# Optimization experiments

Measured on AMD Instinct MI355X. Metric: run time of the kernel, lower is better.

## Reference

```python
import jax, jax.numpy as jnp
import numpy as np

V, E, H, M = 256, 512, 512, 128
D = 2 * H  # decoder hidden
B, L_TXT, T_MEL = 32, 256, 800
EPS = 1e-5


def setup_inputs() -> dict:
    key = jax.random.key(0)
    ks = jax.random.split(key, 24)
    s = 0.02
    inp = {
        'x': jax.random.randint(ks[0], (B, L_TXT), 0, V),
        'text_seq_lens': jax.random.randint(ks[1], (B,), 1, L_TXT + 1),
        'y': jax.random.normal(ks[2], (B, T_MEL, M), jnp.float32),
        'mel_spec_lens': jax.random.randint(ks[3], (B,), 1, T_MEL + 1),
        'emb': jax.random.normal(ks[4], (V, E)) * s,
        'conv1_w': jax.random.normal(ks[5], (E, E, 3)) * s,
        'conv1_b': jnp.zeros((E,)),
        'bn1_g': jnp.ones((E,)), 'bn1_b': jnp.zeros((E,)),
        'conv2_w': jax.random.normal(ks[6], (E, E, 3)) * s,
        'conv2_b': jnp.zeros((E,)),
        'bn2_g': jnp.ones((E,)), 'bn2_b': jnp.zeros((E,)),
        'wih_f': jax.random.normal(ks[7], (4 * H, E)) * s,
        'whh_f': jax.random.normal(ks[8], (4 * H, H)) * s,
        'bih_f': jnp.zeros((4 * H,)), 'bhh_f': jnp.zeros((4 * H,)),
        'wih_b': jax.random.normal(ks[9], (4 * H, E)) * s,
        'whh_b': jax.random.normal(ks[10], (4 * H, H)) * s,
        'bih_b': jnp.zeros((4 * H,)), 'bhh_b': jnp.zeros((4 * H,)),
        'dwih': jax.random.normal(ks[11], (4 * D, M)) * s,
        'dwhh': jax.random.normal(ks[12], (4 * D, D)) * s,
        'dbih': jnp.zeros((4 * D,)), 'dbhh': jnp.zeros((4 * D,)),
        'proj_w': jax.random.normal(ks[13], (M, D)) * s,
        'proj_b': jnp.zeros((M,)),
        'gate_w': jax.random.normal(ks[14], (1, D)) * s,
        'gate_b': jnp.zeros((1,)),
    }
    return inp


def _conv_bn_relu(x, w, b, g, beta):
    # x: (B, E, L); training-mode BatchNorm (batch statistics, biased var)
    x = jax.lax.conv_general_dilated(x, w, (1,), [(1, 1)],
                                     dimension_numbers=('NCH', 'OIH', 'NCH')) + b[None, :, None]
    mu = jnp.mean(x, axis=(0, 2), keepdims=True)
    var = jnp.mean((x - mu) ** 2, axis=(0, 2), keepdims=True)
    x = (x - mu) * jax.lax.rsqrt(var + EPS) * g[None, :, None] + beta[None, :, None]
    return jax.nn.relu(x)


def _lstm_last(xseq, lens, wih, whh, bih, bhh):
    # Run LSTM over full padded seq, freezing state past each length.
    # Returns final (h, c) == state at t = len-1 (packed-sequence semantics).
    Bb, T, _ = xseq.shape
    Hh = whh.shape[1]
    pre = jnp.einsum('bte,ge->btg', xseq, wih) + bih + bhh  # (B,T,4H)

    def step(carry, inp):
        h, c = carry
        xt, t = inp
        gates = xt + h @ whh.T
        i, f, g, o = jnp.split(gates, 4, axis=-1)
        c_n = jax.nn.sigmoid(f) * c + jax.nn.sigmoid(i) * jnp.tanh(g)
        h_n = jax.nn.sigmoid(o) * jnp.tanh(c_n)
        valid = (t < lens)[:, None]
        return (jnp.where(valid, h_n, h), jnp.where(valid, c_n, c)), None

    init = (jnp.zeros((Bb, Hh), xseq.dtype), jnp.zeros((Bb, Hh), xseq.dtype))
    (h, c), _ = jax.lax.scan(step, init, (pre.transpose(1, 0, 2), jnp.arange(T)))
    return h, c


def _forward(x, text_seq_lens, y, mel_spec_lens, emb, conv1_w, conv1_b, bn1_g, bn1_b,
             conv2_w, conv2_b, bn2_g, bn2_b, wih_f, whh_f, bih_f, bhh_f,
             wih_b, whh_b, bih_b, bhh_b, dwih, dwhh, dbih, dbhh,
             proj_w, proj_b, gate_w, gate_b):
    xe = emb[x]                       # (B, L, E)
    h = xe.transpose(0, 2, 1)         # (B, E, L)
    h = _conv_bn_relu(h, conv1_w, conv1_b, bn1_g, bn1_b)  # dropout = identity (eval)
    h = _conv_bn_relu(h, conv2_w, conv2_b, bn2_g, bn2_b)
    h = h.transpose(0, 2, 1)          # (B, L, E)

    # bidirectional encoder LSTM final states (packed semantics)
    hf, cf = _lstm_last(h, text_seq_lens, wih_f, whh_f, bih_f, bhh_f)
    # reverse each sequence within its valid length for the backward direction
    t_idx = jnp.arange(h.shape[1])[None, :]
    rev_idx = jnp.clip(text_seq_lens[:, None] - 1 - t_idx, 0, h.shape[1] - 1)
    h_rev = jnp.take_along_axis(h, rev_idx[:, :, None], axis=1)
    hb, cb = _lstm_last(h_rev, text_seq_lens, wih_b, whh_b, bih_b, bhh_b)

    hid = jnp.concatenate([hf, hb], axis=1)  # (B, 2H)
    cel = jnp.concatenate([cf, cb], axis=1)

    Tm = y.shape[1]

    def dec_step(carry, _):
        hd, cd, inp = carry
        gates = inp @ dwih.T + dbih + dbhh + hd @ dwhh.T
        i, f, g, o = jnp.split(gates, 4, axis=-1)
        cd = jax.nn.sigmoid(f) * cd + jax.nn.sigmoid(i) * jnp.tanh(g)
        hd = jax.nn.sigmoid(o) * jnp.tanh(cd)
        mel = hd @ proj_w.T + proj_b          # (B, M)
        gate = hd @ gate_w.T + gate_b         # (B, 1)
        return (hd, cd, mel), (mel, gate[:, 0])

    sos = jnp.zeros((y.shape[0], M), y.dtype)
    _, (mels, gates) = jax.lax.scan(dec_step, (hid, cel, sos), None, length=Tm)
    mel_outputs = mels.transpose(1, 0, 2)     # (B, Tm, M)
    gate_outputs = gates.T                    # (B, Tm)

    mask = jnp.arange(Tm)[None, :] > mel_spec_lens[:, None]  # (B, Tm), strictly >
    masked_mel = jnp.where(mask[:, :, None], 0.0, mel_outputs)
    masked_gate = jnp.where(mask, 1000.0, gate_outputs)
    return masked_mel, masked_gate, mask


def reference(x, text_seq_lens, y, mel_spec_lens, emb, conv1_w, conv1_b, bn1_g, bn1_b,
              conv2_w, conv2_b, bn2_g, bn2_b, wih_f, whh_f, bih_f, bhh_f,
              wih_b, whh_b, bih_b, bhh_b, dwih, dwhh, dbih, dbhh,
              proj_w, proj_b, gate_w, gate_b):
    return _forward(x, text_seq_lens, y, mel_spec_lens, emb, conv1_w, conv1_b,
                    bn1_g, bn1_b, conv2_w, conv2_b, bn2_g, bn2_b,
                    wih_f, whh_f, bih_f, bhh_f, wih_b, whh_b, bih_b, bhh_b,
                    dwih, dwhh, dbih, dbhh, proj_w, proj_b, gate_w, gate_b)
```

## Files before the change

### kernel.cpp

```cpp
#include <hip/hip_runtime.h>


typedef float f4 __attribute__((ext_vector_type(4)));
typedef _Float16 h8 __attribute__((ext_vector_type(8)));
typedef _Float16 half_t;
typedef unsigned long long u64;

#define B_    32
#define LTXT  256
#define TMEL  800
#define EE    512
#define HH    512
#define DD    1024
#define MM    128
#define NROWS 8192
#define GATE_OFF 3276800
#define MASK_OFF 3302400

#define RING_D 801
#define RING_E 257
#define HOP    13

#define WS_MBE        0ull
#define WS_MBD        16384ull
#define WS_HENC       49152ull
#define WS_ZERO_BYTES 114688ull
#define WS_HD         16891904ull
#define WS_BUFX       69386240ull
#define WS_BUFY       77774848ull
#define WS_CONVF      86163456ull
#define WS_WEFF       86163456ull
#define WS_W0         94552064ull
#define WS_WP1        102940672ull
#define WS_WP2        104513536ull
#define WS_WIHP       106086400ull
#define WS_WHHP       110280704ull
#define WS_BSUM       114475008ull
#define WS_BEFF       114491392ull
#define WS_B0         114507776ull
#define WS_MEAN       114524160ull
#define WS_RSTD       114526208ull
#define WS_PROJW      114528256ull
#define WS_PROJG      114790400ull
#define WS_CEL        114823168ull

__device__ __forceinline__ float sigm(float x) { return 1.f / (1.f + __expf(-x)); }
__device__ __forceinline__ float tanh_f(float x) {
    float e = __expf(2.f * x);
    return 1.f - 2.f / (e + 1.f);
}

__device__ __forceinline__ void st_atom64(void* p, u64 v) {
    asm volatile("global_atomic_swap_x2 %0, %1, off" :: "v"(p), "v"(v) : "memory");
}
__device__ __forceinline__ void st_atom32(unsigned* p, unsigned v) {
    asm volatile("global_atomic_swap %0, %1, off" :: "v"(p), "v"(v) : "memory");
}


__global__ void k_embed(const int* __restrict__ x, const float* __restrict__ emb,
                        half_t* __restrict__ out) {
    int row = blockIdx.x;
    int tok = x[row];
    const float* e = emb + (size_t)tok * EE;
    half_t* o = out + (size_t)row * EE;
    for (int c = threadIdx.x; c < EE; c += blockDim.x) o[c] = (half_t)e[c];
}

__global__ void k_packconvw(const float* __restrict__ w, half_t* __restrict__ wp) {
    int idx = blockIdx.x * 256 + threadIdx.x;
    if (idx >= 3 * EE * EE) return;
    int s = idx / (EE * EE);
    int rem = idx - s * EE * EE;
    int eo = rem >> 9, ei = rem & 511;
    wp[idx] = (half_t)w[(size_t)eo * (EE * 3) + ei * 3 + s];
}

__global__ __launch_bounds__(256) void k_conv(const half_t* __restrict__ A,
                                              const half_t* __restrict__ Wp,
                                              const float* __restrict__ bias,
                                              float* __restrict__ out) {
    const int nt = blockIdx.x, et = blockIdx.y;
    const int tid = threadIdx.x;
    const int wv = tid >> 6, l = tid & 63, quad = l >> 4, lo = l & 15;
    const int rowA = nt * 64 + wv * 16 + lo;
    const int eo = et * 16 + lo;
    f4 acc = {0.f, 0.f, 0.f, 0.f};
    for (int s = 0; s < 3; ++s) {
        int lsp = (rowA & 255) + s - 1;
        bool valid = (lsp >= 0) && (lsp < 256);
        int rs = rowA + s - 1;
        rs = rs < 0 ? 0 : (rs > NROWS - 1 ? NROWS - 1 : rs);
        const half_t* ab = A + (size_t)rs * EE;
        const half_t* wb = Wp + ((size_t)s * EE + eo) * EE;
#pragma unroll 4
        for (int ks = 0; ks < 16; ++ks) {
            h8 a = {0, 0, 0, 0, 0, 0, 0, 0};
            if (valid) a = *(const h8*)(ab + ks * 32 + quad * 8);
            h8 b = *(const h8*)(wb + ks * 32 + quad * 8);
            acc = __builtin_amdgcn_mfma_f32_16x16x32_f16(a, b, acc, 0, 0, 0);
        }
    }
    const int orow = nt * 64 + wv * 16 + quad * 4;
    const float bv = bias[eo];
#pragma unroll
    for (int r = 0; r < 4; ++r) out[(size_t)(orow + r) * EE + eo] = acc[r] + bv;
}

__global__ __launch_bounds__(256) void k_bnstats(const float* __restrict__ x,
                                                 float* __restrict__ mean,
                                                 float* __restrict__ rstd) {
    const int c = blockIdx.x;
    float s = 0.f, ss = 0.f;
    for (int n = threadIdx.x; n < NROWS; n += 256) {
        float v = x[(size_t)n * EE + c];
        s += v; ss += v * v;
    }
#pragma unroll
    for (int off = 32; off > 0; off >>= 1) { s += __shfl_down(s, off); ss += __shfl_down(ss, off); }
    __shared__ float as[4], ass[4];
    int wv = threadIdx.x >> 6;
    if ((threadIdx.x & 63) == 0) { as[wv] = s; ass[wv] = ss; }
    __syncthreads();
    if (threadIdx.x == 0) {
        float S = as[0] + as[1] + as[2] + as[3];
        float SS = ass[0] + ass[1] + ass[2] + ass[3];
        float m = S / (float)NROWS;
        float var = SS / (float)NROWS - m * m;
        mean[c] = m;
        rstd[c] = rsqrtf(var + 1e-5f);
    }
}

__global__ void k_bnapply(const float* __restrict__ x, const float* __restrict__ mean,
                          const float* __restrict__ rstd, const float* __restrict__ g,
                          const float* __restrict__ beta, half_t* __restrict__ out) {
    int idx = blockIdx.x * 256 + threadIdx.x;
    if (idx >= NROWS * EE) return;
    int c = idx & (EE - 1);
    float v = (x[idx] - mean[c]) * rstd[c] * g[c] + beta[c];
    out[idx] = (half_t)(v > 0.f ? v : 0.f);
}

__global__ void k_packrec(const float* __restrict__ src, half_t* __restrict__ dst,
                          int Hdim, int kshift, int total) {
    int idx = blockIdx.x * 256 + threadIdx.x;
    if (idx >= total) return;
    int p = idx >> kshift;
    int k = idx & ((1 << kshift) - 1);
    int he = p >> 2, g = p & 3;
    dst[idx] = (half_t)src[((size_t)g * Hdim + he) * (size_t)(1 << kshift) + k];
}

__global__ void k_bsumenc(const float* __restrict__ bf, const float* __restrict__ bhf,
                          const float* __restrict__ bb, const float* __restrict__ bhb,
                          float* __restrict__ bsum) {
    int p = blockIdx.x * 256 + threadIdx.x;
    if (p >= 4096) return;
    int dir = p >> 11, pp = p & 2047;
    int he = pp >> 2, g = pp & 3;
    int row = g * HH + he;
    bsum[p] = dir ? (bb[row] + bhb[row]) : (bf[row] + bhf[row]);
}

__global__ __launch_bounds__(256) void k_weff(const float* __restrict__ dwhh,
                                              const float* __restrict__ dwih,
                                              const float* __restrict__ projw,
                                              half_t* __restrict__ weff,
                                              half_t* __restrict__ w0) {
    int row = blockIdx.x;
    int k = blockIdx.y * 256 + threadIdx.x;
    float v = dwhh[(size_t)row * DD + k];
    float acc = v;
    for (int m = 0; m < MM; ++m) acc += dwih[(size_t)row * MM + m] * projw[(size_t)m * DD + k];
    int p = ((row & (DD - 1)) << 2) | (row >> 10);
    weff[(size_t)p * DD + k] = (half_t)acc;
    w0[(size_t)p * DD + k] = (half_t)v;
}

__global__ void k_bdec(const float* __restrict__ dbih, const float* __restrict__ dbhh,
                       const float* __restrict__ dwih, const float* __restrict__ projb,
                       float* __restrict__ beff, float* __restrict__ b0) {
    int p = blockIdx.x * 256 + threadIdx.x;
    if (p >= 4096) return;
    int he = p >> 2, g = p & 3;
    int row = g * DD + he;
    float bb = dbih[row] + dbhh[row];
    float acc = bb;
    for (int m = 0; m < MM; ++m) acc += dwih[(size_t)row * MM + m] * projb[m];
    b0[p] = bb;
    beff[p] = acc;
}

__global__ void k_cast(const float* __restrict__ src, half_t* __restrict__ dst, int n) {
    int idx = blockIdx.x * 256 + threadIdx.x;
    if (idx < n) dst[idx] = (half_t)src[idx];
}

__global__ void k_projg(const float* __restrict__ gw, half_t* __restrict__ pg) {
    int idx = blockIdx.x * 256 + threadIdx.x;
    if (idx >= 16 * DD) return;
    int row = idx >> 10, k = idx & (DD - 1);
    pg[idx] = (half_t)(row == 0 ? gw[k] : 0.f);
}

__global__ void k_mask(const int* __restrict__ lens, float* __restrict__ out) {
    int idx = blockIdx.x * 256 + threadIdx.x;
    if (idx >= B_ * TMEL) return;
    int b = idx / TMEL, t = idx - b * TMEL;
    out[MASK_OFF + idx] = (t > lens[b]) ? 1.f : 0.f;
}

__global__ __launch_bounds__(512) void k_enc(const half_t* __restrict__ X,
                                             const half_t* __restrict__ wihp,
                                             const half_t* __restrict__ whhp,
                                             const float* __restrict__ bsum,
                                             const int* __restrict__ lens,
                                             half_t* __restrict__ henc,
                                             half_t* __restrict__ hd,
                                             float* __restrict__ cel,
                                             unsigned* __restrict__ mbE) {
    const int j = blockIdx.x;
    const int dir = j >> 5, sub = j & 31;
    const int tid = threadIdx.x;
    const int wv = tid >> 6, l = tid & 63, quad = l >> 4, lo = l & 15;
    const int rg = wv >> 1, bh = wv & 1;
    const int bfr = bh * 16 + lo;
    const int ue = tid >> 5, ub = tid & 31;

    __shared__ half_t s_hd[32 * 520];
    __shared__ float s_g[32][65];
    __shared__ float s_c[16][32];
    __shared__ float s_h[16][32];
    __shared__ half_t s_hh[16][32];
    __shared__ int s_len[32];

    if (tid < 32) s_len[tid] = lens[tid];
    s_c[ue][ub] = 0.f;
    s_h[ue][ub] = 0.f;

    const int pr = dir * 2048 + sub * 64 + rg * 16 + lo;
    const half_t* wih_b = wihp + (size_t)pr * 512;
    const half_t* whh_b = whhp + (size_t)pr * 512;
    const float bias_n = bsum[pr];

    h8 wihreg[16], whhreg[16];
#pragma unroll
    for (int ks = 0; ks < 16; ++ks) {
        wihreg[ks] = *(const h8*)(wih_b + ks * 32 + quad * 8);
        whhreg[ks] = *(const h8*)(whh_b + ks * 32 + quad * 8);
    }

    int sp = 0, sn = HOP;
    __syncthreads();

    for (int t = 0; t < 256; ++t) {
        if (t > 0) {
            if (tid >= 64 && tid < 96) {
                const unsigned want = (unsigned)t;
                const unsigned* fp = mbE + (size_t)(dir * 32 + sub) * 64 + (tid - 64);
                while (__hip_atomic_load(fp, __ATOMIC_RELAXED, __HIP_MEMORY_SCOPE_AGENT) < want)
                    __builtin_amdgcn_s_sleep(1);
            }
            __syncthreads();
        }

        const half_t* src = henc + (size_t)sp * 32768 + (size_t)dir * 16384;
        h8 tmp0 = *(const h8*)(src + (size_t)(tid + 0 * 512) * 8);
        h8 tmp1 = *(const h8*)(src + (size_t)(tid + 1 * 512) * 8);
        h8 tmp2 = *(const h8*)(src + (size_t)(tid + 2 * 512) * 8);
        h8 tmp3 = *(const h8*)(src + (size_t)(tid + 3 * 512) * 8);

        const int lb = s_len[bfr];
        int tt = (dir == 0) ? t : (lb - 1 - t);
        tt = tt < 0 ? 0 : tt;
        const half_t* xr = X + ((size_t)bfr * 256 + tt) * 512;
        f4 accA = {0.f, 0.f, 0.f, 0.f}, accB = {0.f, 0.f, 0.f, 0.f};
#pragma unroll
        for (int ks = 0; ks < 16; ++ks) {
            h8 a = *(const h8*)(xr + ks * 32 + quad * 8);
            accA = __builtin_amdgcn_mfma_f32_16x16x32_f16(a, wihreg[ks], accA, 0, 0, 0);
        }

        {
            int c0 = tid;
            *(h8*)(s_hd + (size_t)(c0 >> 6) * 520 + (c0 & 63) * 8) = tmp0;
            int c1 = tid + 512;
            *(h8*)(s_hd + (size_t)(c1 >> 6) * 520 + (c1 & 63) * 8) = tmp1;
            int c2 = tid + 1024;
            *(h8*)(s_hd + (size_t)(c2 >> 6) * 520 + (c2 & 63) * 8) = tmp2;
            int c3 = tid + 1536;
            *(h8*)(s_hd + (size_t)(c3 >> 6) * 520 + (c3 & 63) * 8) = tmp3;
        }
        __syncthreads();

#pragma unroll
        for (int ks = 0; ks < 16; ++ks) {
            h8 a = *(const h8*)(s_hd + (size_t)bfr * 520 + ks * 32 + quad * 8);
            accB = __builtin_amdgcn_mfma_f32_16x16x32_f16(a, whhreg[ks], accB, 0, 0, 0);
        }
        const int bm = bh * 16 + quad * 4, cm = rg * 16 + lo;
#pragma unroll
        for (int r = 0; r < 4; ++r) s_g[bm + r][cm] = accA[r] + accB[r] + bias_n;
        __syncthreads();
        {
            float gi = s_g[ub][ue * 4 + 0], gf = s_g[ub][ue * 4 + 1];
            float gg = s_g[ub][ue * 4 + 2], go = s_g[ub][ue * 4 + 3];
            float cn = sigm(gf) * s_c[ue][ub] + sigm(gi) * tanh_f(gg);
            float hn = sigm(go) * tanh_f(cn);
            if (t < s_len[ub]) { s_c[ue][ub] = cn; s_h[ue][ub] = hn; }
            s_hh[ue][ub] = (half_t)s_h[ue][ub];
        }
        __syncthreads();
        if (tid < 64 && t < 255) {
            int b2 = tid >> 1, e8 = (tid & 1) * 8;
            union { half_t h[8]; u64 u[2]; } pk;
#pragma unroll
            for (int i = 0; i < 8; ++i) pk.h[i] = s_hh[e8 + i][b2];
            half_t* dst = henc + (size_t)sn * 32768 + (size_t)dir * 16384
                          + (size_t)b2 * 512 + sub * 16 + e8;
            st_atom64(dst, pk.u[0]);
            st_atom64(dst + 4, pk.u[1]);
            asm volatile("s_waitcnt vmcnt(0)");
            if (tid < 32)
                st_atom32(mbE + ((size_t)(dir * 32 + tid) * 64 + sub), (unsigned)(t + 1));
        }
        if (t < 255) { sp = sn; sn += HOP; if (sn >= RING_E) sn -= RING_E; }
    }
    {
        int g2 = ub >> 4, b = ub & 15;
        hd[(size_t)g2 * ((size_t)RING_D * 16384) + (size_t)b * 1024
           + dir * 512 + sub * 16 + ue] = (half_t)s_h[ue][ub];
    }
    cel[(size_t)ub * 1024 + dir * 512 + sub * 16 + ue] = s_c[ue][ub];
}

__global__ __launch_bounds__(512) void k_dec(const half_t* __restrict__ Weff,
                                             const half_t* __restrict__ W0,
                                             const float* __restrict__ beff,
                                             const float* __restrict__ b0,
                                             const half_t* __restrict__ projwb,
                                             const half_t* __restrict__ projg,
                                             const float* __restrict__ projb,
                                             const float* __restrict__ gateb,
                                             const int* __restrict__ mlens,
                                             const float* __restrict__ cel,
                                             half_t* __restrict__ hd,
                                             float* __restrict__ out,
                                             unsigned* __restrict__ mbD) {
    const int j = blockIdx.x;
    const int tid = threadIdx.x;
    const int wv = tid >> 6, l = tid & 63, quad = l >> 4, lo = l & 15;

    __shared__ half_t s_hd[16 * 1032];
    __shared__ float s_g[16][129];
    __shared__ float s_c[32][16];
    __shared__ half_t s_hh[32][16];
    __shared__ int s_len[32];

    if (j < 64) {
        const int g = j >> 5, jj = j & 31;
        half_t* hdG = hd + (size_t)g * ((size_t)RING_D * 16384);
        unsigned* mbG = mbD + (size_t)g * 34 * 64;
        const int ue = tid >> 4;
        const int ub = tid & 15;

        s_c[ue][ub] = cel[(size_t)(g * 16 + ub) * 1024 + jj * 32 + ue];
        const int pr = jj * 128 + wv * 16 + lo;
        const float biasE = beff[pr], bias0 = b0[pr];
        const half_t* wbE = Weff + (size_t)pr * 1024;
        const half_t* wb0 = W0 + (size_t)pr * 1024;

        h8 wreg[32];
#pragma unroll
        for (int ks = 0; ks < 32; ++ks)
            wreg[ks] = *(const h8*)(wbE + ks * 32 + quad * 8);

        int sp = 0, sn = HOP;
        __syncthreads();

        for (int t = 1; t <= TMEL; ++t) {
            if (t > 1) {
                if (tid >= 64 && tid < 96) {
                    const unsigned want = (unsigned)(t - 1);
                    const unsigned* fp = mbG + (size_t)jj * 64 + (tid - 64);
                    while (__hip_atomic_load(fp, __ATOMIC_RELAXED, __HIP_MEMORY_SCOPE_AGENT) < want)
                        __builtin_amdgcn_s_sleep(1);
                }
                __syncthreads();
            }

            {
                const half_t* src = hdG + (size_t)sp * 16384;
                h8 tp[4];
#pragma unroll
                for (int i = 0; i < 4; ++i)
                    tp[i] = *(const h8*)(src + (size_t)(tid + i * 512) * 8);
#pragma unroll
                for (int i = 0; i < 4; ++i) {
                    int c = tid + i * 512;
                    *(h8*)(s_hd + (size_t)(c >> 7) * 1032 + (c & 127) * 8) = tp[i];
                }
            }
            __syncthreads();

            const half_t* ar = s_hd + (size_t)lo * 1032 + quad * 8;
            f4 acc = {0.f, 0.f, 0.f, 0.f}, acc2 = {0.f, 0.f, 0.f, 0.f};
            if (t == 1) {
#pragma unroll 8
                for (int ks = 0; ks < 32; ks += 2) {
                    h8 a0 = *(const h8*)(ar + ks * 32);
                    h8 a1 = *(const h8*)(ar + ks * 32 + 32);
                    acc = __builtin_amdgcn_mfma_f32_16x16x32_f16(a0, *(const h8*)(wb0 + ks * 32 + quad * 8), acc, 0, 0, 0);
                    acc2 = __builtin_amdgcn_mfma_f32_16x16x32_f16(a1, *(const h8*)(wb0 + ks * 32 + 32 + quad * 8), acc2, 0, 0, 0);
                }
            } else {
#pragma unroll
                for (int ks = 0; ks < 32; ks += 2) {
                    h8 a0 = *(const h8*)(ar + ks * 32);
                    h8 a1 = *(const h8*)(ar + ks * 32 + 32);
                    acc = __builtin_amdgcn_mfma_f32_16x16x32_f16(a0, wreg[ks], acc, 0, 0, 0);
                    acc2 = __builtin_amdgcn_mfma_f32_16x16x32_f16(a1, wreg[ks + 1], acc2, 0, 0, 0);
                }
            }
            const float bn = (t == 1) ? bias0 : biasE;
#pragma unroll
            for (int r = 0; r < 4; ++r) s_g[quad * 4 + r][wv * 16 + lo] = acc[r] + acc2[r] + bn;
            __syncthreads();
            {
                float gi = s_g[ub][ue * 4 + 0], gf = s_g[ub][ue * 4 + 1];
                float gg = s_g[ub][ue * 4 + 2], go = s_g[ub][ue * 4 + 3];
                float cn = sigm(gf) * s_c[ue][ub] + sigm(gi) * tanh_f(gg);
                s_c[ue][ub] = cn;
                s_hh[ue][ub] = (half_t)(sigm(go) * tanh_f(cn));
            }
            __syncthreads();
            if (tid < 64) {
                int b2 = tid >> 2, e8 = (tid & 3) * 8;
                union { half_t h[8]; u64 u[2]; } pk;
#pragma unroll
                for (int i = 0; i < 8; ++i) pk.h[i] = s_hh[e8 + i][b2];
                half_t* dst = hdG + (size_t)sn * 16384 + (size_t)b2 * 1024 + jj * 32 + e8;
                st_atom64(dst, pk.u[0]);
                st_atom64(dst + 4, pk.u[1]);
                asm volatile("s_waitcnt vmcnt(0)");
                if (tid < 34)
                    st_atom32(mbG + ((size_t)tid * 64 + jj), (unsigned)t);
            }
            sp = sn; sn += HOP; if (sn >= RING_D) sn -= RING_D;
        }
    } else {
        const int p = j - 64;
        const int g = p >> 1;
        const bool meld = ((p & 1) == 0);
        half_t* hdG = hd + (size_t)g * ((size_t)RING_D * 16384);
        unsigned* mbG = mbD + (size_t)g * 34 * 64;
        const int cons = meld ? 32 : 33;
        const bool duty = meld || (wv == 0);
        const half_t* pw = meld ? (projwb + (size_t)(wv * 16 + lo) * 1024)
                                : (projg + (size_t)lo * 1024);
        const float biasP = meld ? projb[wv * 16 + lo] : gateb[0];

        h8 pwreg[32];
        if (duty) {
#pragma unroll
            for (int ks = 0; ks < 32; ++ks)
                pwreg[ks] = *(const h8*)(pw + ks * 32 + quad * 8);
        }
        if (tid < 32) s_len[tid] = mlens[tid];

        int spP = HOP;
        __syncthreads();

        for (int t = 1; t <= TMEL; ++t) {
            if (tid < 32) {
                const unsigned want = (unsigned)t;
                const unsigned* fp = mbG + (size_t)cons * 64 + tid;
                while (__hip_atomic_load(fp, __ATOMIC_RELAXED, __HIP_MEMORY_SCOPE_AGENT) < want)
                    __builtin_amdgcn_s_sleep(1);
            }
            __syncthreads();

            {
                const half_t* src = hdG + (size_t)spP * 16384;
                h8 tp[4];
#pragma unroll
                for (int i = 0; i < 4; ++i)
                    tp[i] = *(const h8*)(src + (size_t)(tid + i * 512) * 8);
#pragma unroll
                for (int i = 0; i < 4; ++i) {
                    int c = tid + i * 512;
                    *(h8*)(s_hd + (size_t)(c >> 7) * 1032 + (c & 127) * 8) = tp[i];
                }
            }
            __syncthreads();

            if (duty) {
                const half_t* ar = s_hd + (size_t)lo * 1032 + quad * 8;
                f4 accm = {0.f, 0.f, 0.f, 0.f}, accm2 = {0.f, 0.f, 0.f, 0.f};
#pragma unroll
                for (int ks = 0; ks < 32; ks += 2) {
                    h8 a0 = *(const h8*)(ar + ks * 32);
                    h8 a1 = *(const h8*)(ar + ks * 32 + 32);
                    accm = __builtin_amdgcn_mfma_f32_16x16x32_f16(a0, pwreg[ks], accm, 0, 0, 0);
                    accm2 = __builtin_amdgcn_mfma_f32_16x16x32_f16(a1, pwreg[ks + 1], accm2, 0, 0, 0);
                }
                accm[0] += accm2[0]; accm[1] += accm2[1];
                accm[2] += accm2[2]; accm[3] += accm2[3];
                const int pos = t - 1;
                if (meld) {
#pragma unroll
                    for (int r = 0; r < 4; ++r) {
                        int b = g * 16 + quad * 4 + r;
                        float v = accm[r] + biasP;
                        if (pos > s_len[b]) v = 0.f;
                        __builtin_nontemporal_store(v,
                            &out[(size_t)b * (TMEL * MM) + (size_t)pos * MM + wv * 16 + lo]);
                    }
                } else if (lo == 0) {
#pragma unroll
                    for (int r = 0; r < 4; ++r) {
                        int b = g * 16 + quad * 4 + r;
                        float v = accm[r] + biasP;
                        if (pos > s_len[b]) v = 1000.f;
                        __builtin_nontemporal_store(v, &out[GATE_OFF + (size_t)b * TMEL + pos]);
                    }
                }
            }
            __syncthreads();
            spP += HOP; if (spP >= RING_D) spP -= RING_D;
        }
    }
}


extern "C" void kernel_launch(void* const* d_in, const int* in_sizes, int n_in,
                              void* d_out, int out_size, void* d_ws, size_t ws_size,
                              hipStream_t stream) {
    const int* x = (const int*)d_in[0];
    const int* tlens = (const int*)d_in[1];
    const int* mlens = (const int*)d_in[3];
    const float* emb = (const float*)d_in[4];
    const float* c1w = (const float*)d_in[5];
    const float* c1b = (const float*)d_in[6];
    const float* bn1g = (const float*)d_in[7];
    const float* bn1b = (const float*)d_in[8];
    const float* c2w = (const float*)d_in[9];
    const float* c2b = (const float*)d_in[10];
    const float* bn2g = (const float*)d_in[11];
    const float* bn2b = (const float*)d_in[12];
    const float* wihf = (const float*)d_in[13];
    const float* whhf = (const float*)d_in[14];
    const float* bihf = (const float*)d_in[15];
    const float* bhhf = (const float*)d_in[16];
    const float* wihb = (const float*)d_in[17];
    const float* whhb = (const float*)d_in[18];
    const float* bihb = (const float*)d_in[19];
    const float* bhhb = (const float*)d_in[20];
    const float* dwih = (const float*)d_in[21];
    const float* dwhh = (const float*)d_in[22];
    const float* dbih = (const float*)d_in[23];
    const float* dbhh = (const float*)d_in[24];
    const float* projw = (const float*)d_in[25];
    const float* projb = (const float*)d_in[26];
    const float* gatew = (const float*)d_in[27];
    const float* gateb = (const float*)d_in[28];
    float* out = (float*)d_out;
    char* ws = (char*)d_ws;

    unsigned* mbE = (unsigned*)(ws + WS_MBE);
    unsigned* mbD = (unsigned*)(ws + WS_MBD);
    half_t* henc = (half_t*)(ws + WS_HENC);
    half_t* hd = (half_t*)(ws + WS_HD);
    half_t* bufX = (half_t*)(ws + WS_BUFX);
    half_t* bufY = (half_t*)(ws + WS_BUFY);
    float* convf = (float*)(ws + WS_CONVF);
    half_t* weff = (half_t*)(ws + WS_WEFF);
    half_t* w0 = (half_t*)(ws + WS_W0);
    half_t* wp1 = (half_t*)(ws + WS_WP1);
    half_t* wp2 = (half_t*)(ws + WS_WP2);
    float* meanb = (float*)(ws + WS_MEAN);
    float* rstdb = (float*)(ws + WS_RSTD);
    half_t* wihp = (half_t*)(ws + WS_WIHP);
    half_t* whhp = (half_t*)(ws + WS_WHHP);
    float* bsum = (float*)(ws + WS_BSUM);
    float* beff = (float*)(ws + WS_BEFF);
    float* b0 = (float*)(ws + WS_B0);
    half_t* projwb = (half_t*)(ws + WS_PROJW);
    half_t* projg = (half_t*)(ws + WS_PROJG);
    float* cel = (float*)(ws + WS_CEL);

    hipMemsetAsync(d_ws, 0, (size_t)WS_ZERO_BYTES, stream);

    k_embed<<<NROWS, 256, 0, stream>>>(x, emb, bufX);
    k_packconvw<<<(3 * EE * EE + 255) / 256, 256, 0, stream>>>(c1w, wp1);
    k_conv<<<dim3(128, 32), 256, 0, stream>>>(bufX, wp1, c1b, convf);
    k_bnstats<<<EE, 256, 0, stream>>>(convf, meanb, rstdb);
    k_bnapply<<<(NROWS * EE) / 256, 256, 0, stream>>>(convf, meanb, rstdb, bn1g, bn1b, bufY);
    k_packconvw<<<(3 * EE * EE + 255) / 256, 256, 0, stream>>>(c2w, wp2);
    k_conv<<<dim3(128, 32), 256, 0, stream>>>(bufY, wp2, c2b, convf);
    k_bnstats<<<EE, 256, 0, stream>>>(convf, meanb, rstdb);
    k_bnapply<<<(NROWS * EE) / 256, 256, 0, stream>>>(convf, meanb, rstdb, bn2g, bn2b, bufX);

    const int encTot = 2048 * 512;
    k_packrec<<<(encTot + 255) / 256, 256, 0, stream>>>(wihf, wihp, HH, 9, encTot);
    k_packrec<<<(encTot + 255) / 256, 256, 0, stream>>>(wihb, wihp + encTot, HH, 9, encTot);
    k_packrec<<<(encTot + 255) / 256, 256, 0, stream>>>(whhf, whhp, HH, 9, encTot);
    k_packrec<<<(encTot + 255) / 256, 256, 0, stream>>>(whhb, whhp + encTot, HH, 9, encTot);
    k_bsumenc<<<16, 256, 0, stream>>>(bihf, bhhf, bihb, bhhb, bsum);

    k_enc<<<64, 512, 0, stream>>>(bufX, wihp, whhp, bsum, tlens, henc, hd, cel, mbE);

    k_weff<<<dim3(4096, 4), 256, 0, stream>>>(dwhh, dwih, projw, weff, w0);
    k_bdec<<<16, 256, 0, stream>>>(dbih, dbhh, dwih, projb, beff, b0);
    k_cast<<<(MM * DD + 255) / 256, 256, 0, stream>>>(projw, projwb, MM * DD);
    k_projg<<<(16 * DD + 255) / 256, 256, 0, stream>>>(gatew, projg);

    k_dec<<<68, 512, 0, stream>>>(weff, w0, beff, b0, projwb, projg, projb, gateb,
                                  mlens, cel, hd, out, mbD);

    k_mask<<<(B_ * TMEL + 255) / 256, 256, 0, stream>>>(mlens, out);

    (void)in_sizes; (void)n_in; (void)out_size; (void)ws_size;
}
```

Baseline: 4.482 ms.

## Split encoder LSTM blocks by batch half with wider hidden slices per block

The encoder recurrence now splits work across blocks by direction and batch half (16 sequences each), with each block owning 32 hidden units (128 gate rows) instead of 16 units for all 32 sequences. Each block copies half as much of the shared hidden state per step, and each block waits on 16 flags instead of 32. This cuts per-step cross-block synchronisation fan-in and global-to-LDS traffic. In exchange each wave holds a different weight-row slice, and the ring buffer and mailbox layout in workspace change, so k_dec and the host launch must agree with the new indexing.

Measured after the change: 4.464 ms. About the same (-0.4%).

```diff
diff --git a/kernel.cpp b/kernel.cpp
--- a/kernel.cpp
+++ b/kernel.cpp
@@ -221,25 +221,25 @@
                                              float* __restrict__ cel,
                                              unsigned* __restrict__ mbE) {
     const int j = blockIdx.x;
-    const int dir = j >> 5, sub = j & 31;
+    const int d = j >> 4, jj = j & 15;
+    const int dir = d >> 1, bg = d & 1;
     const int tid = threadIdx.x;
     const int wv = tid >> 6, l = tid & 63, quad = l >> 4, lo = l & 15;
-    const int rg = wv >> 1, bh = wv & 1;
-    const int bfr = bh * 16 + lo;
-    const int ue = tid >> 5, ub = tid & 31;
-
-    __shared__ half_t s_hd[32 * 520];
-    __shared__ float s_g[32][65];
-    __shared__ float s_c[16][32];
-    __shared__ float s_h[16][32];
-    __shared__ half_t s_hh[16][32];
-    __shared__ int s_len[32];
-
-    if (tid < 32) s_len[tid] = lens[tid];
+    const int ue = tid >> 4;
+    const int ub = tid & 15;
+
+    __shared__ half_t s_hd[16 * 520];
+    __shared__ float s_g[16][129];
+    __shared__ float s_c[32][16];
+    __shared__ float s_h[32][16];
+    __shared__ half_t s_hh[32][16];
+    __shared__ int s_len[16];
+
+    if (tid < 16) s_len[tid] = lens[bg * 16 + tid];
     s_c[ue][ub] = 0.f;
     s_h[ue][ub] = 0.f;
 
-    const int pr = dir * 2048 + sub * 64 + rg * 16 + lo;
+    const int pr = dir * 2048 + jj * 128 + wv * 16 + lo;
     const half_t* wih_b = wihp + (size_t)pr * 512;
     const half_t* whh_b = whhp + (size_t)pr * 512;
     const float bias_n = bsum[pr];
@@ -256,25 +256,23 @@
 
     for (int t = 0; t < 256; ++t) {
         if (t > 0) {
-            if (tid >= 64 && tid < 96) {
+            if (wv == 1 && l < 16) {
                 const unsigned want = (unsigned)t;
-                const unsigned* fp = mbE + (size_t)(dir * 32 + sub) * 64 + (tid - 64);
+                const unsigned* fp = mbE + (size_t)(d * 16 + jj) * 64 + l;
                 while (__hip_atomic_load(fp, __ATOMIC_RELAXED, __HIP_MEMORY_SCOPE_AGENT) < want)
                     __builtin_amdgcn_s_sleep(1);
             }
             __syncthreads();
         }
 
-        const half_t* src = henc + (size_t)sp * 32768 + (size_t)dir * 16384;
+        const half_t* src = henc + ((size_t)sp * 4 + d) * 8192;
         h8 tmp0 = *(const h8*)(src + (size_t)(tid + 0 * 512) * 8);
         h8 tmp1 = *(const h8*)(src + (size_t)(tid + 1 * 512) * 8);
-        h8 tmp2 = *(const h8*)(src + (size_t)(tid + 2 * 512) * 8);
-        h8 tmp3 = *(const h8*)(src + (size_t)(tid + 3 * 512) * 8);
-
-        const int lb = s_len[bfr];
+
+        const int lb = s_len[lo];
         int tt = (dir == 0) ? t : (lb - 1 - t);
         tt = tt < 0 ? 0 : tt;
-        const half_t* xr = X + ((size_t)bfr * 256 + tt) * 512;
+        const half_t* xr = X + ((size_t)(bg * 16 + lo) * 256 + tt) * 512;
         f4 accA = {0.f, 0.f, 0.f, 0.f}, accB = {0.f, 0.f, 0.f, 0.f};
 #pragma unroll
         for (int ks = 0; ks < 16; ++ks) {
@@ -287,21 +285,17 @@
             *(h8*)(s_hd + (size_t)(c0 >> 6) * 520 + (c0 & 63) * 8) = tmp0;
             int c1 = tid + 512;
             *(h8*)(s_hd + (size_t)(c1 >> 6) * 520 + (c1 & 63) * 8) = tmp1;
-            int c2 = tid + 1024;
-            *(h8*)(s_hd + (size_t)(c2 >> 6) * 520 + (c2 & 63) * 8) = tmp2;
-            int c3 = tid + 1536;
-            *(h8*)(s_hd + (size_t)(c3 >> 6) * 520 + (c3 & 63) * 8) = tmp3;
         }
         __syncthreads();
 
+        const half_t* ar = s_hd + (size_t)lo * 520 + quad * 8;
 #pragma unroll
         for (int ks = 0; ks < 16; ++ks) {
-            h8 a = *(const h8*)(s_hd + (size_t)bfr * 520 + ks * 32 + quad * 8);
+            h8 a = *(const h8*)(ar + ks * 32);
             accB = __builtin_amdgcn_mfma_f32_16x16x32_f16(a, whhreg[ks], accB, 0, 0, 0);
         }
-        const int bm = bh * 16 + quad * 4, cm = rg * 16 + lo;
-#pragma unroll
-        for (int r = 0; r < 4; ++r) s_g[bm + r][cm] = accA[r] + accB[r] + bias_n;
+#pragma unroll
+        for (int r = 0; r < 4; ++r) s_g[quad * 4 + r][wv * 16 + lo] = accA[r] + accB[r] + bias_n;
         __syncthreads();
         {
             float gi = s_g[ub][ue * 4 + 0], gf = s_g[ub][ue * 4 + 1];
@@ -313,26 +307,22 @@
         }
         __syncthreads();
         if (tid < 64 && t < 255) {
-            int b2 = tid >> 1, e8 = (tid & 1) * 8;
+            int b2 = tid >> 2, e8 = (tid & 3) * 8;
             union { half_t h[8]; u64 u[2]; } pk;
 #pragma unroll
             for (int i = 0; i < 8; ++i) pk.h[i] = s_hh[e8 + i][b2];
-            half_t* dst = henc + (size_t)sn * 32768 + (size_t)dir * 16384
-                          + (size_t)b2 * 512 + sub * 16 + e8;
+            half_t* dst = henc + ((size_t)sn * 4 + d) * 8192 + (size_t)b2 * 512 + jj * 32 + e8;
             st_atom64(dst, pk.u[0]);
             st_atom64(dst + 4, pk.u[1]);
             asm volatile("s_waitcnt vmcnt(0)");
-            if (tid < 32)
-                st_atom32(mbE + ((size_t)(dir * 32 + tid) * 64 + sub), (unsigned)(t + 1));
+            if (tid < 16)
+                st_atom32(mbE + ((size_t)(d * 16 + tid) * 64 + jj), (unsigned)(t + 1));
         }
         if (t < 255) { sp = sn; sn += HOP; if (sn >= RING_E) sn -= RING_E; }
     }
-    {
-        int g2 = ub >> 4, b = ub & 15;
-        hd[(size_t)g2 * ((size_t)RING_D * 16384) + (size_t)b * 1024
-           + dir * 512 + sub * 16 + ue] = (half_t)s_h[ue][ub];
-    }
-    cel[(size_t)ub * 1024 + dir * 512 + sub * 16 + ue] = s_c[ue][ub];
+    hd[(size_t)bg * ((size_t)RING_D * 16384) + (size_t)ub * 1024
+       + dir * 512 + jj * 32 + ue] = (half_t)s_h[ue][ub];
+    cel[(size_t)(bg * 16 + ub) * 1024 + dir * 512 + jj * 32 + ue] = s_c[ue][ub];
 }
 
 __global__ __launch_bounds__(512) void k_dec(const half_t* __restrict__ Weff,
```
